# Performance work log

Measured on AMD Instinct MI355X. Metric: run time of the kernel, lower is better.

## Reference

```python
import jax, jax.numpy as jnp
import numpy as np

DN = ('NCHW', 'OIHW', 'NCHW')
LAP = jnp.array([[0., -1., 0.], [-1., 4., -1.], [0., -1., 0.]], dtype=jnp.float32).reshape(1, 1, 3, 3)
CH, NE = 24, 256


def conv(x, w, stride=1, pad=0):
    return jax.lax.conv_general_dilated(x, w, (stride, stride), ((pad, pad), (pad, pad)), dimension_numbers=DN)


def conv_t(x, w):
    # torch ConvTranspose2d(k=4, s=2, p=1); w is torch layout [in, out, 4, 4]
    wt = jnp.flip(w, (2, 3)).transpose(1, 0, 2, 3)
    return jax.lax.conv_general_dilated(x, wt, (1, 1), ((2, 2), (2, 2)), lhs_dilation=(2, 2), dimension_numbers=DN)


def spatial_attn(x, w_sa):
    y = jnp.concatenate([jnp.mean(x, 1, keepdims=True), jnp.max(x, 1, keepdims=True)], 1)
    return x * jax.nn.sigmoid(conv(y, w_sa, pad=3))


def res_branch(x, wr, wp, wsa):
    k = wr.shape[-1]
    h = conv(x, wr, pad=k // 2)
    h = conv(h, wp)
    return jax.nn.relu(spatial_attn(h, wsa))


def enc_block(x, wr, wp, wsa, wout):
    x = x + res_branch(x, wr, wp, wsa)
    return conv(x, wout, stride=2, pad=1)


def dec_block(x, wr, wp, wsa, wout):
    x = conv_t(x, wout)
    return x + res_branch(x, wr, wp, wsa)


def quantize(inp, embed):
    # inp: [B,H,W,D] tokens, embed: [D,N] codebook
    f = inp.reshape(-1, inp.shape[-1])
    dist = (f * f).sum(1, keepdims=True) - 2.0 * (f @ embed) + (embed * embed).sum(0, keepdims=True)
    ind = jnp.argmin(dist, axis=1)
    q = jnp.take(embed.T, ind, axis=0).reshape(inp.shape)
    diff = jnp.mean((jax.lax.stop_gradient(q) - inp) ** 2)
    q = inp + jax.lax.stop_gradient(q - inp)  # straight-through
    return q, diff


def _forward(x, w_img_in, w_img_out,
             w_res_et, w_pw_et, w_sa_et, w_out_et,
             w_res_em, w_pw_em, w_sa_em, w_out_em,
             w_res_ed, w_pw_ed, w_sa_ed, w_out_ed,
             w_res_dt, w_pw_dt, w_sa_dt, w_out_dt,
             w_res_dm, w_pw_dm, w_sa_dm, w_out_dm,
             w_res_dd, w_pw_dd, w_sa_dd, w_out_dd,
             w_squ1, w_squ2, embed2, embed3):
    xl = jax.lax.stop_gradient(conv(jnp.mean(x, 1, keepdims=True), LAP, pad=1))
    h = conv(xl, w_img_in)
    enc1 = enc_block(h, w_res_et, w_pw_et, w_sa_et, w_out_et)      # H/2
    enc2 = enc_block(enc1, w_res_em, w_pw_em, w_sa_em, w_out_em)   # H/4
    enc3 = enc_block(enc2, w_res_ed, w_pw_ed, w_sa_ed, w_out_ed)   # H/8
    qt2, d2 = quantize(enc2.transpose(0, 2, 3, 1), embed2)
    qt2 = qt2.transpose(0, 3, 1, 2)
    qt3, d3 = quantize(enc3.transpose(0, 2, 3, 1), embed3)
    qt3 = qt3.transpose(0, 3, 1, 2)
    dec3 = dec_block(qt3, w_res_dd, w_pw_dd, w_sa_dd, w_out_dd)    # H/4
    dec2 = conv(jnp.concatenate([dec3, qt2], 1), w_squ2)
    dec2 = dec_block(dec2, w_res_dm, w_pw_dm, w_sa_dm, w_out_dm)   # H/2
    dec1 = conv(jnp.concatenate([dec2, enc1], 1), w_squ1)
    dec1 = dec_block(dec1, w_res_dt, w_pw_dt, w_sa_dt, w_out_dt)   # H
    mask_lap = conv(dec1, w_img_out)
    clean_lap = xl - mask_lap
    return mask_lap, clean_lap, (d2 + d3).reshape(1)


def _param_shapes():
    shapes = {'w_img_in': (CH, 1, 1, 1), 'w_img_out': (1, CH, 1, 1),
              'w_squ1': (CH, 2 * CH, 1, 1), 'w_squ2': (CH, 2 * CH, 1, 1),
              'embed2': (CH, NE), 'embed3': (CH, NE)}
    for tag, k in [('et', 7), ('em', 5), ('ed', 3), ('dt', 7), ('dm', 5), ('dd', 3)]:
        shapes['w_res_' + tag] = (CH, CH, k, k)
        shapes['w_pw_' + tag] = (CH, CH, 1, 1)
        shapes['w_sa_' + tag] = (1, 2, 7, 7)
        shapes['w_out_' + tag] = (CH, CH, 4, 4)
    return shapes


def setup_inputs() -> dict:
    key = jax.random.key(0)
    shapes = _param_shapes()
    names = sorted(shapes)
    keys = jax.random.split(key, len(names) + 1)
    inputs = {'x': jax.random.normal(keys[0], (8, 3, 512, 512), dtype=jnp.float32)}
    for k_, name in zip(keys[1:], names):
        w = jax.random.normal(k_, shapes[name], dtype=jnp.float32)
        if not name.startswith('embed'):
            w = w * 0.05  # conv weight init scale
        inputs[name] = w
    return inputs


def reference(x, embed2, embed3, w_img_in, w_img_out,
              w_out_dd, w_out_dm, w_out_dt, w_out_ed, w_out_em, w_out_et,
              w_pw_dd, w_pw_dm, w_pw_dt, w_pw_ed, w_pw_em, w_pw_et,
              w_res_dd, w_res_dm, w_res_dt, w_res_ed, w_res_em, w_res_et,
              w_sa_dd, w_sa_dm, w_sa_dt, w_sa_ed, w_sa_em, w_sa_et,
              w_squ1, w_squ2):
    return _forward(x, w_img_in, w_img_out,
                    w_res_et, w_pw_et, w_sa_et, w_out_et,
                    w_res_em, w_pw_em, w_sa_em, w_out_em,
                    w_res_ed, w_pw_ed, w_sa_ed, w_out_ed,
                    w_res_dt, w_pw_dt, w_sa_dt, w_out_dt,
                    w_res_dm, w_pw_dm, w_sa_dm, w_out_dm,
                    w_res_dd, w_pw_dd, w_sa_dd, w_out_dd,
                    w_squ1, w_squ2, embed2, embed3)
```

## Files before the change

### kernel.cpp

```cpp
#include <hip/hip_runtime.h>
#include <math.h>

#define CH 24

typedef __attribute__((ext_vector_type(8))) short short8v;
typedef __attribute__((ext_vector_type(4))) float f32x4;
typedef unsigned short ushort_t;
typedef unsigned int uint_t;

__device__ inline ushort_t bf16r(float f){
  uint_t u = __float_as_uint(f);
  u += 0x7FFF + ((u>>16)&1);
  return (ushort_t)(u>>16);
}
__device__ inline float bf2f(uint_t u){ return __uint_as_float(u<<16); }

__global__ void k_r_pw(const float* __restrict__ w, float* __restrict__ wT, int CIN){
  int i = blockIdx.x*256 + threadIdx.x;
  if (i >= CIN*24) return;
  int co = i % 24, ci = i/24;
  wT[i] = w[co*CIN+ci];
}
__global__ void k_rmfma(const float* __restrict__ w, ushort_t* __restrict__ wb, int K){
  int i = blockIdx.x*256 + threadIdx.x;
  int n = K*K*1024; if (i >= n) return;
  int j = i & 7, l = (i>>3) & 63, t = (i>>9) & 1, tap = i >> 10;
  int ci = (l>>4)*8 + j, co = t*16 + (l&15);
  int ky = tap / K, kx = tap % K;
  float v = (ci<24 && co<24) ? w[((co*24+ci)*K+ky)*K+kx] : 0.f;
  wb[i] = bf16r(v);
}
__global__ void k_rmfma4(const float* __restrict__ w, ushort_t* __restrict__ wb){
  int i = blockIdx.x*256 + threadIdx.x;
  if (i >= 16384) return;
  int j = i & 7, l = (i>>3) & 63, t = (i>>9) & 1, tap = i >> 10;
  int ci = (l>>4)*8 + j, co = t*16 + (l&15);
  int ky = tap >> 2, kx = tap & 3;
  float v = (ci<24 && co<24) ? w[((ci*24+co)*4+ky)*4+kx] : 0.f;
  wb[i] = bf16r(v);
}


__global__ void k_lap(const float* __restrict__ x, float* __restrict__ xl, int H, int W){
  int idx = blockIdx.x*256 + threadIdx.x;
  int HW = H*W;
  if (idx >= HW) return;
  const float* xb = x + (size_t)blockIdx.z*3*HW;
  float* xo = xl + (size_t)blockIdx.z*HW;
  int px = idx % W, py = idx / W;
#define MEANV(yy,xx) (((yy)>=0&&(yy)<H&&(xx)>=0&&(xx)<W) ? (xb[(yy)*W+(xx)]+xb[HW+(yy)*W+(xx)]+xb[2*HW+(yy)*W+(xx)])*(1.f/3.f) : 0.f)
  float v = 4.f*MEANV(py,px) - MEANV(py-1,px) - MEANV(py+1,px) - MEANV(py,px-1) - MEANV(py,px+1);
#undef MEANV
  xo[idx] = v;
}

template<int K, bool EXPAND, bool INBF, bool OUTBF>
__launch_bounds__(512)
__global__ void k_conv_mfma(const void* in, const ushort_t* __restrict__ wb,
                            const ushort_t* __restrict__ wbpw, const float* __restrict__ wexp,
                            void* out, float* __restrict__ mm,
                            int H, int W, int istrIn, int istrOut, int istrMM){
  constexpr int SW_T = 32 + K - 1;
  constexpr int SH = 16 + K - 1;
  constexpr int NPX = SH*SW_T;
  __shared__ ushort_t lds[NPX*24];
  __shared__ uint_t sc[8][16*20];
  int tid = threadIdx.x;
  const float* inb_f = (const float*)in + (size_t)blockIdx.z*istrIn;
  const ushort_t* inb_b = (const ushort_t*)in + (size_t)blockIdx.z*istrIn;
  int x0g = blockIdx.x*32 - K/2, y0g = blockIdx.y*16 - K/2;
  int HW = H*W;
  for (int i = tid; i < NPX*3; i += 512){
    int q = i / NPX;
    int pp = i - q*NPX;
    int row = pp / SW_T, col = pp - row*SW_T;
    int gy = y0g + row, gx = x0g + col;
    uint4 w4; w4.x=0u; w4.y=0u; w4.z=0u; w4.w=0u;
    if (gy >= 0 && gy < H && gx >= 0 && gx < W){
      size_t base = (size_t)gy*W + gx;
      int c0 = q*8;
      if (EXPAND){
        float val = inb_f[base];
        w4.x = (uint_t)bf16r(val*wexp[c0+0]) | ((uint_t)bf16r(val*wexp[c0+1])<<16);
        w4.y = (uint_t)bf16r(val*wexp[c0+2]) | ((uint_t)bf16r(val*wexp[c0+3])<<16);
        w4.z = (uint_t)bf16r(val*wexp[c0+4]) | ((uint_t)bf16r(val*wexp[c0+5])<<16);
        w4.w = (uint_t)bf16r(val*wexp[c0+6]) | ((uint_t)bf16r(val*wexp[c0+7])<<16);
      } else if (INBF){
        uint_t u0=inb_b[(size_t)(c0+0)*HW+base], u1=inb_b[(size_t)(c0+1)*HW+base];
        uint_t u2=inb_b[(size_t)(c0+2)*HW+base], u3=inb_b[(size_t)(c0+3)*HW+base];
        uint_t u4=inb_b[(size_t)(c0+4)*HW+base], u5=inb_b[(size_t)(c0+5)*HW+base];
        uint_t u6=inb_b[(size_t)(c0+6)*HW+base], u7=inb_b[(size_t)(c0+7)*HW+base];
        w4.x = u0 | (u1<<16); w4.y = u2 | (u3<<16); w4.z = u4 | (u5<<16); w4.w = u6 | (u7<<16);
      } else {
        w4.x = (uint_t)bf16r(inb_f[(size_t)(c0+0)*HW+base]) | ((uint_t)bf16r(inb_f[(size_t)(c0+1)*HW+base])<<16);
        w4.y = (uint_t)bf16r(inb_f[(size_t)(c0+2)*HW+base]) | ((uint_t)bf16r(inb_f[(size_t)(c0+3)*HW+base])<<16);
        w4.z = (uint_t)bf16r(inb_f[(size_t)(c0+4)*HW+base]) | ((uint_t)bf16r(inb_f[(size_t)(c0+5)*HW+base])<<16);
        w4.w = (uint_t)bf16r(inb_f[(size_t)(c0+6)*HW+base]) | ((uint_t)bf16r(inb_f[(size_t)(c0+7)*HW+base])<<16);
      }
    }
    *(uint4*)(lds + (size_t)pp*24 + q*8) = w4;
  }
  __syncthreads();
  int l = tid & 63, wid = tid >> 6;
  int kg = l >> 4, li = l & 15;
  int kgc = (kg < 3) ? kg : 2;
  f32x4 zero = {0.f,0.f,0.f,0.f};
  f32x4 acc[4][2];
  #pragma unroll
  for (int i=0;i<4;i++){ acc[i][0]=zero; acc[i][1]=zero; }

  const ushort_t* aln = lds + li*24 + kgc*8 + (size_t)wid*SW_T*24;

  #pragma unroll
  for (int ky=0; ky<K; ky++){
    #pragma unroll
    for (int kx=0; kx<K; kx++){
      int tap = ky*K + kx;
      const ushort_t* wp = wb + (size_t)tap*1024;
      short8v b0 = *(const short8v*)(wp + l*8);
      short8v b1 = *(const short8v*)(wp + 512 + l*8);
      #pragma unroll
      for (int i=0;i<4;i++){
        const ushort_t* ap = aln + (((i&1)*8 + ky)*SW_T + (i>>1)*16 + kx)*24;
        short8v a = *(const short8v*)ap;
        acc[i][0] = __builtin_amdgcn_mfma_f32_16x16x32_bf16(a, b0, acc[i][0], 0, 0, 0);
        acc[i][1] = __builtin_amdgcn_mfma_f32_16x16x32_bf16(a, b1, acc[i][1], 0, 0, 0);
      }
    }
  }
  short8v bpw0 = *(const short8v*)(wbpw + l*8);
  short8v bpw1 = *(const short8v*)(wbpw + 512 + l*8);
  uint_t* s = sc[wid];
  float* outb_f = (float*)out + (size_t)blockIdx.z*istrOut;
  ushort_t* outb_b = (ushort_t*)out + (size_t)blockIdx.z*istrOut;
  float* mmb = mm + (size_t)blockIdx.z*istrMM;
  #pragma unroll 1
  for (int i=0;i<4;i++){
    __asm__ volatile("s_waitcnt lgkmcnt(0)" ::: "memory");
    __builtin_amdgcn_sched_barrier(0);
    #pragma unroll
    for (int reg=0; reg<4; reg++){
      float v0 = acc[i][0][reg], v1 = acc[i][1][reg];
      float v0n = __shfl_xor(v0, 1, 64);
      float v1n = __shfl_xor(v1, 1, 64);
      int pxr = kg*4 + reg;
      uint_t packed; int uidx;
      if ((li & 1) == 0){
        packed = (uint_t)bf16r(v0) | ((uint_t)bf16r(v0n) << 16);
        uidx = li >> 1;
      } else {
        packed = (uint_t)bf16r(v1n) | ((uint_t)bf16r(v1) << 16);
        uidx = 8 + (li >> 1);
      }
      s[pxr*20 + uidx] = packed;
    }
    __asm__ volatile("s_waitcnt lgkmcnt(0)" ::: "memory");
    __builtin_amdgcn_sched_barrier(0);
    short8v a2 = *(const short8v*)((const ushort_t*)s + li*40 + kg*8);
    f32x4 d0 = __builtin_amdgcn_mfma_f32_16x16x32_bf16(a2, bpw0, zero, 0, 0, 0);
    f32x4 d1 = __builtin_amdgcn_mfma_f32_16x16x32_bf16(a2, bpw1, zero, 0, 0, 0);
    int gy = blockIdx.y*16 + wid + (i&1)*8;
    int gx = blockIdx.x*32 + (i>>1)*16 + kg*4;
    if (OUTBF){
      uint2 p0; p0.x = (uint_t)bf16r(d0[0]) | ((uint_t)bf16r(d0[1])<<16);
      p0.y = (uint_t)bf16r(d0[2]) | ((uint_t)bf16r(d0[3])<<16);
      *(uint2*)(outb_b + (size_t)li*HW + (size_t)gy*W + gx) = p0;
      if (li < 8){
        uint2 p1; p1.x = (uint_t)bf16r(d1[0]) | ((uint_t)bf16r(d1[1])<<16);
        p1.y = (uint_t)bf16r(d1[2]) | ((uint_t)bf16r(d1[3])<<16);
        *(uint2*)(outb_b + (size_t)(16+li)*HW + (size_t)gy*W + gx) = p1;
      }
    } else {
      *(f32x4*)(outb_f + (size_t)li*HW + (size_t)gy*W + gx) = d0;
      if (li < 8)
        *(f32x4*)(outb_f + (size_t)(16+li)*HW + (size_t)gy*W + gx) = d1;
    }
    f32x4 sm, mx;
    #pragma unroll
    for (int reg=0; reg<4; reg++){
      sm[reg] = d0[reg] + d1[reg];
      mx[reg] = fmaxf(d0[reg], (li<8) ? d1[reg] : -3.4e38f);
    }
    #pragma unroll
    for (int m=1; m<16; m<<=1){
      #pragma unroll
      for (int reg=0; reg<4; reg++){
        sm[reg] += __shfl_xor(sm[reg], m, 64);
        mx[reg] = fmaxf(mx[reg], __shfl_xor(mx[reg], m, 64));
      }
    }
    if (li == 0){
      f32x4 me; me[0]=sm[0]*(1.f/24.f); me[1]=sm[1]*(1.f/24.f); me[2]=sm[2]*(1.f/24.f); me[3]=sm[3]*(1.f/24.f);
      *(f32x4*)(mmb + (size_t)gy*W + gx) = me;
      *(f32x4*)(mmb + (size_t)HW + (size_t)gy*W + gx) = mx;
    }
  }
}

template<bool INBF, bool OUTBF>
__launch_bounds__(512)
__global__ void k_convT_mfma(const void* in, const ushort_t* __restrict__ wb,
                             void* out, int Ho, int Wo, int istrIn, int istrOut){
  const int Hi = Ho>>1, Wi = Wo>>1;
  constexpr int SW_T = 18, NPX = 180;
  __shared__ ushort_t lds[NPX*24];
  int tid = threadIdx.x;
  const float* inb_f = (const float*)in + (size_t)blockIdx.z*istrIn;
  const ushort_t* inb_b = (const ushort_t*)in + (size_t)blockIdx.z*istrIn;
  int X0 = blockIdx.x*32, Y0 = blockIdx.y*16;
  int ix0 = (X0>>1) - 1, iy0 = (Y0>>1) - 1;
  int HWi = Hi*Wi;
  for (int i = tid; i < NPX*3; i += 512){
    int q = i / NPX;
    int pp = i - q*NPX;
    int row = pp / SW_T, col = pp - row*SW_T;
    int gy = iy0 + row, gx = ix0 + col;
    uint4 w4; w4.x=0u; w4.y=0u; w4.z=0u; w4.w=0u;
    if (gy>=0 && gy<Hi && gx>=0 && gx<Wi){
      size_t base = (size_t)gy*Wi + gx;
      int c0 = q*8;
      if (INBF){
        uint_t u0=inb_b[(size_t)(c0+0)*HWi+base], u1=inb_b[(size_t)(c0+1)*HWi+base];
        uint_t u2=inb_b[(size_t)(c0+2)*HWi+base], u3=inb_b[(size_t)(c0+3)*HWi+base];
        uint_t u4=inb_b[(size_t)(c0+4)*HWi+base], u5=inb_b[(size_t)(c0+5)*HWi+base];
        uint_t u6=inb_b[(size_t)(c0+6)*HWi+base], u7=inb_b[(size_t)(c0+7)*HWi+base];
        w4.x = u0 | (u1<<16); w4.y = u2 | (u3<<16); w4.z = u4 | (u5<<16); w4.w = u6 | (u7<<16);
      } else {
        w4.x = (uint_t)bf16r(inb_f[(size_t)(c0+0)*HWi+base]) | ((uint_t)bf16r(inb_f[(size_t)(c0+1)*HWi+base])<<16);
        w4.y = (uint_t)bf16r(inb_f[(size_t)(c0+2)*HWi+base]) | ((uint_t)bf16r(inb_f[(size_t)(c0+3)*HWi+base])<<16);
        w4.z = (uint_t)bf16r(inb_f[(size_t)(c0+4)*HWi+base]) | ((uint_t)bf16r(inb_f[(size_t)(c0+5)*HWi+base])<<16);
        w4.w = (uint_t)bf16r(inb_f[(size_t)(c0+6)*HWi+base]) | ((uint_t)bf16r(inb_f[(size_t)(c0+7)*HWi+base])<<16);
      }
    }
    *(uint4*)(lds + (size_t)pp*24 + q*8) = w4;
  }
  __syncthreads();
  int l = tid & 63, wid = tid >> 6;
  int kg = l >> 4, li = l & 15;
  int kgc = (kg < 3) ? kg : 2;
  f32x4 zero = {0.f,0.f,0.f,0.f};
  f32x4 acc[4][2];
  #pragma unroll
  for (int i=0;i<4;i++){ acc[i][0]=zero; acc[i][1]=zero; }

  const ushort_t* aln = lds + li*24 + kgc*8;

  #pragma unroll
  for (int i=0;i<4;i++){
    int g = wid + 8*i;
    int r = g & 15, q = g >> 4;
    int ky0 = (r+1)&1;
    #pragma unroll
    for (int t2=0;t2<2;t2++){
      int ky = ky0 + 2*t2;
      int liy = ((r+1-ky)>>1) + 1;
      #pragma unroll
      for (int u=0;u<2;u++){
        int kx = (q ? 0 : 1) + 2*u;
        int lixb = ((q+1-kx)>>1) + 1;
        int tap = ky*4 + kx;
        const ushort_t* wp = wb + (size_t)tap*1024;
        short8v b0 = *(const short8v*)(wp + l*8);
        short8v b1 = *(const short8v*)(wp + 512 + l*8);
        short8v a = *(const short8v*)(aln + (liy*SW_T + lixb)*24);
        acc[i][0] = __builtin_amdgcn_mfma_f32_16x16x32_bf16(a, b0, acc[i][0], 0, 0, 0);
        acc[i][1] = __builtin_amdgcn_mfma_f32_16x16x32_bf16(a, b1, acc[i][1], 0, 0, 0);
      }
    }
  }
  float* outb_f = (float*)out + (size_t)blockIdx.z*istrOut;
  ushort_t* outb_b = (ushort_t*)out + (size_t)blockIdx.z*istrOut;
  int HWo = Ho*Wo;
  #pragma unroll
  for (int i=0;i<4;i++){
    int g = wid + 8*i;
    int r = g & 15, q = g >> 4;
    int oy = Y0 + r;
    #pragma unroll
    for (int reg=0; reg<4; reg++){
      int ox = X0 + 2*(kg*4 + reg) + q;
      if (OUTBF){
        outb_b[(size_t)li*HWo + (size_t)oy*Wo + ox] = bf16r(acc[i][0][reg]);
        if (li < 8)
          outb_b[(size_t)(16+li)*HWo + (size_t)oy*Wo + ox] = bf16r(acc[i][1][reg]);
      } else {
        outb_f[(size_t)li*HWo + (size_t)oy*Wo + ox] = acc[i][0][reg];
        if (li < 8)
          outb_f[(size_t)(16+li)*HWo + (size_t)oy*Wo + ox] = acc[i][1][reg];
      }
    }
  }
}

template<bool INBF, bool OUTBF>
__launch_bounds__(512)
__global__ void k_down_mfma(const void* in, const ushort_t* __restrict__ wb,
                            void* out, int Ho, int Wo, int istrIn, int istrOut){
  const int Hi = Ho*2, Wi = Wo*2;
  constexpr int NPX = 18*34;
  __shared__ ushort_t lds[NPX*24];
  int tid = threadIdx.x;
  const float* inb_f = (const float*)in + (size_t)blockIdx.z*istrIn;
  const ushort_t* inb_b = (const ushort_t*)in + (size_t)blockIdx.z*istrIn;
  int X0 = blockIdx.x*16, Y0 = blockIdx.y*8;
  int ix0 = 2*X0 - 1, iy0 = 2*Y0 - 1;
  int HWi = Hi*Wi;
  for (int i = tid; i < NPX*3; i += 512){
    int q = i / NPX;
    int pp = i - q*NPX;
    int row = pp / 34;
    int rem = pp - row*34;
    int par = (rem >= 17) ? 1 : 0;
    int sub = rem - par*17;
    int gx = ix0 + 2*sub + par;
    int gy = iy0 + row;
    uint4 w4; w4.x=0u; w4.y=0u; w4.z=0u; w4.w=0u;
    if (gy>=0 && gy<Hi && gx>=0 && gx<Wi){
      size_t base = (size_t)gy*Wi + gx;
      int c0 = q*8;
      if (INBF){
        uint_t u0=inb_b[(size_t)(c0+0)*HWi+base], u1=inb_b[(size_t)(c0+1)*HWi+base];
        uint_t u2=inb_b[(size_t)(c0+2)*HWi+base], u3=inb_b[(size_t)(c0+3)*HWi+base];
        uint_t u4=inb_b[(size_t)(c0+4)*HWi+base], u5=inb_b[(size_t)(c0+5)*HWi+base];
        uint_t u6=inb_b[(size_t)(c0+6)*HWi+base], u7=inb_b[(size_t)(c0+7)*HWi+base];
        w4.x = u0 | (u1<<16); w4.y = u2 | (u3<<16); w4.z = u4 | (u5<<16); w4.w = u6 | (u7<<16);
      } else {
        w4.x = (uint_t)bf16r(inb_f[(size_t)(c0+0)*HWi+base]) | ((uint_t)bf16r(inb_f[(size_t)(c0+1)*HWi+base])<<16);
        w4.y = (uint_t)bf16r(inb_f[(size_t)(c0+2)*HWi+base]) | ((uint_t)bf16r(inb_f[(size_t)(c0+3)*HWi+base])<<16);
        w4.z = (uint_t)bf16r(inb_f[(size_t)(c0+4)*HWi+base]) | ((uint_t)bf16r(inb_f[(size_t)(c0+5)*HWi+base])<<16);
        w4.w = (uint_t)bf16r(inb_f[(size_t)(c0+6)*HWi+base]) | ((uint_t)bf16r(inb_f[(size_t)(c0+7)*HWi+base])<<16);
      }
    }
    *(uint4*)(lds + (size_t)pp*24 + q*8) = w4;
  }
  __syncthreads();
  int l = tid & 63, wid = tid >> 6;
  int kg = l >> 4, li = l & 15;
  int kgc = (kg < 3) ? kg : 2;
  f32x4 zero = {0.f,0.f,0.f,0.f};
  f32x4 acc0 = zero, acc1 = zero;
  const ushort_t* aln = lds + li*24 + kgc*8 + (size_t)(2*wid)*34*24;
  #pragma unroll
  for (int ky=0; ky<4; ky++){
    #pragma unroll
    for (int kx=0; kx<4; kx++){
      int tap = ky*4 + kx;
      const ushort_t* wp = wb + (size_t)tap*1024;
      short8v b0 = *(const short8v*)(wp + l*8);
      short8v b1 = *(const short8v*)(wp + 512 + l*8);
      short8v a = *(const short8v*)(aln + (ky*34 + (kx&1)*17 + (kx>>1))*24);
      acc0 = __builtin_amdgcn_mfma_f32_16x16x32_bf16(a, b0, acc0, 0, 0, 0);
      acc1 = __builtin_amdgcn_mfma_f32_16x16x32_bf16(a, b1, acc1, 0, 0, 0);
    }
  }
  int HWo = Ho*Wo;
  int oy = Y0 + wid, ox = X0 + kg*4;
  if (OUTBF){
    ushort_t* outb = (ushort_t*)out + (size_t)blockIdx.z*istrOut;
    uint2 p0; p0.x = (uint_t)bf16r(acc0[0]) | ((uint_t)bf16r(acc0[1])<<16);
    p0.y = (uint_t)bf16r(acc0[2]) | ((uint_t)bf16r(acc0[3])<<16);
    *(uint2*)(outb + (size_t)li*HWo + (size_t)oy*Wo + ox) = p0;
    if (li < 8){
      uint2 p1; p1.x = (uint_t)bf16r(acc1[0]) | ((uint_t)bf16r(acc1[1])<<16);
      p1.y = (uint_t)bf16r(acc1[2]) | ((uint_t)bf16r(acc1[3])<<16);
      *(uint2*)(outb + (size_t)(16+li)*HWo + (size_t)oy*Wo + ox) = p1;
    }
  } else {
    float* outb = (float*)out + (size_t)blockIdx.z*istrOut;
    *(f32x4*)(outb + (size_t)li*HWo + (size_t)oy*Wo + ox) = acc0;
    if (li < 8)
      *(f32x4*)(outb + (size_t)(16+li)*HWo + (size_t)oy*Wo + ox) = acc1;
  }
}

template<bool BF>
__global__ void k_attn_res(const void* R_, const float* __restrict__ M,
                           const void* X_, const float* __restrict__ wsa,
                           void* out_, int H, int W, int istr, int istrMM){
  int p = (blockIdx.x*256 + threadIdx.x)*4;
  int HW = H*W;
  if (p >= HW) return;
  int py = p / W, px0 = p % W;
  const float* Mb = M + (size_t)blockIdx.z*istrMM;
  float s[4]={0,0,0,0};
  #pragma unroll
  for (int cc=0;cc<2;cc++){
    const float* Mc = Mb + (size_t)cc*HW;
    #pragma unroll 1
    for (int ky=0;ky<7;ky++){
      int gy = py+ky-3;
      if (gy<0||gy>=H) continue;
      const float* mr = Mc + (size_t)gy*W;
      float mv[10];
      #pragma unroll
      for (int j=0;j<10;j++){
        int gx = px0-3+j;
        mv[j] = (gx>=0 && gx<W) ? mr[gx] : 0.f;
      }
      const float* wr = wsa + (cc*7+ky)*7;
      #pragma unroll
      for (int kx=0;kx<7;kx++){
        float wv = wr[kx];
        #pragma unroll
        for (int px=0;px<4;px++) s[px] = fmaf(mv[kx+px], wv, s[px]);
      }
    }
  }
  float g[4];
  #pragma unroll
  for (int px=0;px<4;px++) g[px] = 1.f/(1.f+expf(-s[px]));
  #pragma unroll
  for (int c=0;c<CH;c++){
    float r0,r1,r2,r3, x0v,x1v,x2v,x3v;
    if (BF){
      const ushort_t* Rb = (const ushort_t*)R_ + (size_t)blockIdx.z*istr + (size_t)c*HW + p;
      const ushort_t* Xb = (const ushort_t*)X_ + (size_t)blockIdx.z*istr + (size_t)c*HW + p;
      uint2 rv = *(const uint2*)Rb;
      uint2 xv = *(const uint2*)Xb;
      r0=bf2f(rv.x&0xffffu); r1=bf2f(rv.x>>16); r2=bf2f(rv.y&0xffffu); r3=bf2f(rv.y>>16);
      x0v=bf2f(xv.x&0xffffu); x1v=bf2f(xv.x>>16); x2v=bf2f(xv.y&0xffffu); x3v=bf2f(xv.y>>16);
    } else {
      const float* Rb = (const float*)R_ + (size_t)blockIdx.z*istr + (size_t)c*HW + p;
      const float* Xb = (const float*)X_ + (size_t)blockIdx.z*istr + (size_t)c*HW + p;
      float4 rv = *(const float4*)Rb;
      float4 xv = *(const float4*)Xb;
      r0=rv.x; r1=rv.y; r2=rv.z; r3=rv.w;
      x0v=xv.x; x1v=xv.y; x2v=xv.z; x3v=xv.w;
    }
    float o0 = x0v + fmaxf(r0*g[0], 0.f);
    float o1 = x1v + fmaxf(r1*g[1], 0.f);
    float o2 = x2v + fmaxf(r2*g[2], 0.f);
    float o3 = x3v + fmaxf(r3*g[3], 0.f);
    if (BF){
      ushort_t* Ob = (ushort_t*)out_ + (size_t)blockIdx.z*istr + (size_t)c*HW + p;
      uint2 ov;
      ov.x = (uint_t)bf16r(o0) | ((uint_t)bf16r(o1)<<16);
      ov.y = (uint_t)bf16r(o2) | ((uint_t)bf16r(o3)<<16);
      *(uint2*)Ob = ov;
    } else {
      float* Ob = (float*)out_ + (size_t)blockIdx.z*istr + (size_t)c*HW + p;
      float4 ov; ov.x=o0; ov.y=o1; ov.z=o2; ov.w=o3;
      *(float4*)Ob = ov;
    }
  }
}

template<bool BF>
__global__ void k_attn_res_x(const void* R_, const float* __restrict__ M,
                             const float* __restrict__ XL, const float* __restrict__ wsa,
                             const float* __restrict__ wexp,
                             void* out_, int H, int W, int istr, int istrMM){
  int p = (blockIdx.x*256 + threadIdx.x)*4;
  int HW = H*W;
  if (p >= HW) return;
  int py = p / W, px0 = p % W;
  const float* Mb = M + (size_t)blockIdx.z*istrMM;
  float s[4]={0,0,0,0};
  #pragma unroll
  for (int cc=0;cc<2;cc++){
    const float* Mc = Mb + (size_t)cc*HW;
    #pragma unroll 1
    for (int ky=0;ky<7;ky++){
      int gy = py+ky-3;
      if (gy<0||gy>=H) continue;
      const float* mr = Mc + (size_t)gy*W;
      float mv[10];
      #pragma unroll
      for (int j=0;j<10;j++){
        int gx = px0-3+j;
        mv[j] = (gx>=0 && gx<W) ? mr[gx] : 0.f;
      }
      const float* wr = wsa + (cc*7+ky)*7;
      #pragma unroll
      for (int kx=0;kx<7;kx++){
        float wv = wr[kx];
        #pragma unroll
        for (int px=0;px<4;px++) s[px] = fmaf(mv[kx+px], wv, s[px]);
      }
    }
  }
  float g[4];
  #pragma unroll
  for (int px=0;px<4;px++) g[px] = 1.f/(1.f+expf(-s[px]));
  float4 xl4 = *(const float4*)(XL + (size_t)blockIdx.z*HW + p);
  #pragma unroll
  for (int c=0;c<CH;c++){
    float wc = wexp[c];
    float r0,r1,r2,r3;
    if (BF){
      const ushort_t* Rb = (const ushort_t*)R_ + (size_t)blockIdx.z*istr + (size_t)c*HW + p;
      uint2 rv = *(const uint2*)Rb;
      r0=bf2f(rv.x&0xffffu); r1=bf2f(rv.x>>16); r2=bf2f(rv.y&0xffffu); r3=bf2f(rv.y>>16);
    } else {
      const float* Rb = (const float*)R_ + (size_t)blockIdx.z*istr + (size_t)c*HW + p;
      float4 rv = *(const float4*)Rb;
      r0=rv.x; r1=rv.y; r2=rv.z; r3=rv.w;
    }
    float o0 = xl4.x*wc + fmaxf(r0*g[0], 0.f);
    float o1 = xl4.y*wc + fmaxf(r1*g[1], 0.f);
    float o2 = xl4.z*wc + fmaxf(r2*g[2], 0.f);
    float o3 = xl4.w*wc + fmaxf(r3*g[3], 0.f);
    if (BF){
      ushort_t* Ob = (ushort_t*)out_ + (size_t)blockIdx.z*istr + (size_t)c*HW + p;
      uint2 ov;
      ov.x = (uint_t)bf16r(o0) | ((uint_t)bf16r(o1)<<16);
      ov.y = (uint_t)bf16r(o2) | ((uint_t)bf16r(o3)<<16);
      *(uint2*)Ob = ov;
    } else {
      float* Ob = (float*)out_ + (size_t)blockIdx.z*istr + (size_t)c*HW + p;
      float4 ov; ov.x=o0; ov.y=o1; ov.z=o2; ov.w=o3;
      *(float4*)Ob = ov;
    }
  }
}

__global__ void k_attn_final(const ushort_t* __restrict__ R, const float* __restrict__ M,
                             const ushort_t* __restrict__ X, const float* __restrict__ wsa,
                             const float* __restrict__ wout, const float* __restrict__ xl,
                             float* __restrict__ outMask, float* __restrict__ outClean,
                             int H, int W, int istr, int istrMM){
  int p = (blockIdx.x*256 + threadIdx.x)*4;
  int HW = H*W;
  if (p >= HW) return;
  int py = p / W, px0 = p % W;
  const float* Mb = M + (size_t)blockIdx.z*istrMM;
  float s[4]={0,0,0,0};
  #pragma unroll
  for (int cc=0;cc<2;cc++){
    const float* Mc = Mb + (size_t)cc*HW;
    #pragma unroll 1
    for (int ky=0;ky<7;ky++){
      int gy = py+ky-3;
      if (gy<0||gy>=H) continue;
      const float* mr = Mc + (size_t)gy*W;
      float mv[10];
      #pragma unroll
      for (int j=0;j<10;j++){
        int gx = px0-3+j;
        mv[j] = (gx>=0 && gx<W) ? mr[gx] : 0.f;
      }
      const float* wr = wsa + (cc*7+ky)*7;
      #pragma unroll
      for (int kx=0;kx<7;kx++){
        float wv = wr[kx];
        #pragma unroll
        for (int px=0;px<4;px++) s[px] = fmaf(mv[kx+px], wv, s[px]);
      }
    }
  }
  float g[4];
  #pragma unroll
  for (int px=0;px<4;px++) g[px] = 1.f/(1.f+expf(-s[px]));
  float m0=0.f,m1=0.f,m2=0.f,m3=0.f;
  #pragma unroll
  for (int c=0;c<CH;c++){
    const ushort_t* Rb = R + (size_t)blockIdx.z*istr + (size_t)c*HW + p;
    const ushort_t* Xb = X + (size_t)blockIdx.z*istr + (size_t)c*HW + p;
    uint2 rv = *(const uint2*)Rb;
    uint2 xv = *(const uint2*)Xb;
    float wc = wout[c];
    float o0 = bf2f(xv.x&0xffffu) + fmaxf(bf2f(rv.x&0xffffu)*g[0], 0.f);
    float o1 = bf2f(xv.x>>16)     + fmaxf(bf2f(rv.x>>16)*g[1], 0.f);
    float o2 = bf2f(xv.y&0xffffu) + fmaxf(bf2f(rv.y&0xffffu)*g[2], 0.f);
    float o3 = bf2f(xv.y>>16)     + fmaxf(bf2f(rv.y>>16)*g[3], 0.f);
    m0 = fmaf(o0,wc,m0); m1 = fmaf(o1,wc,m1); m2 = fmaf(o2,wc,m2); m3 = fmaf(o3,wc,m3);
  }
  float4 xlv = *(const float4*)(xl + (size_t)blockIdx.z*HW + p);
  float4 mo; mo.x=m0; mo.y=m1; mo.z=m2; mo.w=m3;
  float4 co; co.x=xlv.x-m0; co.y=xlv.y-m1; co.z=xlv.z-m2; co.w=xlv.w-m3;
  *(float4*)(outMask + (size_t)blockIdx.z*HW + p) = mo;
  *(float4*)(outClean + (size_t)blockIdx.z*HW + p) = co;
}

template<bool BF>
__global__ void k_squeeze(const void* inA_, const void* inB_,
                          const float* __restrict__ wT, void* out_, int HW, int istr){
  int p = (blockIdx.x*256 + threadIdx.x)*4;
  if (p >= HW) return;
  float acc[CH][4];
  #pragma unroll
  for (int co=0;co<CH;co++){ acc[co][0]=0;acc[co][1]=0;acc[co][2]=0;acc[co][3]=0; }
  #pragma unroll 1
  for (int ci=0;ci<48;ci++){
    float v0,v1,v2,v3;
    if (BF){
      const ushort_t* src = (ci<24)
        ? ((const ushort_t*)inA_ + (size_t)blockIdx.z*istr + (size_t)ci*HW + p)
        : ((const ushort_t*)inB_ + (size_t)blockIdx.z*istr + (size_t)(ci-24)*HW + p);
      uint2 rv = *(const uint2*)src;
      v0=bf2f(rv.x&0xffffu); v1=bf2f(rv.x>>16); v2=bf2f(rv.y&0xffffu); v3=bf2f(rv.y>>16);
    } else {
      const float* src = (ci<24)
        ? ((const float*)inA_ + (size_t)blockIdx.z*istr + (size_t)ci*HW + p)
        : ((const float*)inB_ + (size_t)blockIdx.z*istr + (size_t)(ci-24)*HW + p);
      float4 rv = *(const float4*)src;
      v0=rv.x; v1=rv.y; v2=rv.z; v3=rv.w;
    }
    const float* wp = wT + ci*24;
    #pragma unroll
    for (int co=0;co<CH;co++){
      float wv = wp[co];
      acc[co][0] = fmaf(v0, wv, acc[co][0]);
      acc[co][1] = fmaf(v1, wv, acc[co][1]);
      acc[co][2] = fmaf(v2, wv, acc[co][2]);
      acc[co][3] = fmaf(v3, wv, acc[co][3]);
    }
  }
  #pragma unroll
  for (int co=0;co<CH;co++){
    if (BF){
      ushort_t* ob = (ushort_t*)out_ + (size_t)blockIdx.z*istr + (size_t)co*HW + p;
      uint2 ov;
      ov.x = (uint_t)bf16r(acc[co][0]) | ((uint_t)bf16r(acc[co][1])<<16);
      ov.y = (uint_t)bf16r(acc[co][2]) | ((uint_t)bf16r(acc[co][3])<<16);
      *(uint2*)ob = ov;
    } else {
      float* ob = (float*)out_ + (size_t)blockIdx.z*istr + (size_t)co*HW + p;
      float4 o; o.x=acc[co][0]; o.y=acc[co][1]; o.z=acc[co][2]; o.w=acc[co][3];
      *(float4*)ob = o;
    }
  }
}

__global__ void k_quant(const float* __restrict__ enc, const float* __restrict__ embed,
                        float* __restrict__ qt, float* __restrict__ diffAcc, int HW, int istr){
  __shared__ float em[256*28];
  __shared__ float red[4];
  {
    int j = threadIdx.x;
    float s = 0.f;
    #pragma unroll
    for (int c=0;c<CH;c++){
      float e = embed[c*256+j];
      em[j*28+c] = -2.0f*e;
      s = fmaf(e,e,s);
    }
    em[j*28+24] = s; em[j*28+25]=0.f; em[j*28+26]=0.f; em[j*28+27]=0.f;
  }
  __syncthreads();
  int p = blockIdx.x*256 + threadIdx.x;
  const float* eb = enc + (size_t)blockIdx.z*istr;
  float f[CH];
  #pragma unroll
  for (int c=0;c<CH;c++) f[c] = eb[(size_t)c*HW + p];
  float best = 3.4e38f; int bj = 0;
  #pragma unroll 1
  for (int j=0;j<256;j++){
    const float4* row = (const float4*)&em[j*28];
    float s = em[j*28+24];
    #pragma unroll
    for (int q4=0;q4<6;q4++){
      float4 r = row[q4];
      s = fmaf(f[q4*4+0], r.x, s);
      s = fmaf(f[q4*4+1], r.y, s);
      s = fmaf(f[q4*4+2], r.z, s);
      s = fmaf(f[q4*4+3], r.w, s);
    }
    if (s < best){ best = s; bj = j; }
  }
  float* qb = qt + (size_t)blockIdx.z*istr;
  float d = 0.f;
  #pragma unroll
  for (int c=0;c<CH;c++){
    float q = embed[c*256+bj];
    qb[(size_t)c*HW + p] = q;
    float e = q - f[c];
    d = fmaf(e,e,d);
  }
  #pragma unroll
  for (int off=32; off>0; off>>=1) d += __shfl_down(d, off, 64);
  int lane = threadIdx.x & 63, wv = threadIdx.x >> 6;
  if (lane==0) red[wv] = d;
  __syncthreads();
  if (threadIdx.x==0) atomicAdd(diffAcc, red[0]+red[1]+red[2]+red[3]);
}

__global__ void k_diff(const float* __restrict__ acc, float* __restrict__ out){
  out[0] = acc[0]*(1.f/3145728.f) + acc[1]*(1.f/786432.f);
}

extern "C" void kernel_launch(void* const* d_in, const int* in_sizes, int n_in,
                              void* d_out, int out_size, void* d_ws, size_t ws_size,
                              hipStream_t stream) {
  const float* x        = (const float*)d_in[0];
  const float* embed2   = (const float*)d_in[1];
  const float* embed3   = (const float*)d_in[2];
  const float* w_img_in = (const float*)d_in[3];
  const float* w_img_out= (const float*)d_in[4];
  const float* w_out_dd = (const float*)d_in[5];
  const float* w_out_dm = (const float*)d_in[6];
  const float* w_out_dt = (const float*)d_in[7];
  const float* w_out_ed = (const float*)d_in[8];
  const float* w_out_em = (const float*)d_in[9];
  const float* w_out_et = (const float*)d_in[10];
  const float* w_pw_dd  = (const float*)d_in[11];
  const float* w_pw_dm  = (const float*)d_in[12];
  const float* w_pw_dt  = (const float*)d_in[13];
  const float* w_pw_ed  = (const float*)d_in[14];
  const float* w_pw_em  = (const float*)d_in[15];
  const float* w_pw_et  = (const float*)d_in[16];
  const float* w_res_dd = (const float*)d_in[17];
  const float* w_res_dm = (const float*)d_in[18];
  const float* w_res_dt = (const float*)d_in[19];
  const float* w_res_ed = (const float*)d_in[20];
  const float* w_res_em = (const float*)d_in[21];
  const float* w_res_et = (const float*)d_in[22];
  const float* w_sa_dd  = (const float*)d_in[23];
  const float* w_sa_dm  = (const float*)d_in[24];
  const float* w_sa_dt  = (const float*)d_in[25];
  const float* w_sa_ed  = (const float*)d_in[26];
  const float* w_sa_em  = (const float*)d_in[27];
  const float* w_sa_et  = (const float*)d_in[28];
  const float* w_squ1   = (const float*)d_in[29];
  const float* w_squ2   = (const float*)d_in[30];
  (void)in_sizes; (void)n_in; (void)out_size;

  const int HW512 = 512*512, HW256 = 256*256, HW128 = 128*128, HW64 = 64*64;
  const int S512 = 24*HW512, S256 = 24*HW256, S128 = 24*HW128, S64 = 24*HW64;

  float* ws = (float*)d_ws;
  float* OUT = (float*)d_out;
  size_t F = ws_size / sizeof(float);

  float* WT      = ws;
  float* wt_squ1 = WT + 154368;
  float* wt_squ2 = WT + 155520;

  ushort_t* WB = (ushort_t*)(ws + 160000);
  ushort_t* wb_et7   = WB;
  ushort_t* wb_dt7   = WB + 50176;
  ushort_t* wb_em5   = WB + 100352;
  ushort_t* wb_dm5   = WB + 125952;
  ushort_t* wb_pw_et = WB + 151552;
  ushort_t* wb_pw_em = WB + 152576;
  ushort_t* wb_pw_dm = WB + 153600;
  ushort_t* wb_pw_dt = WB + 154624;
  ushort_t* wb4_dd   = WB + 155648;
  ushort_t* wb4_dm   = WB + 172032;
  ushort_t* wb4_dt   = WB + 188416;
  ushort_t* wb4d_et  = WB + 204800;
  ushort_t* wb4d_em  = WB + 221184;
  ushort_t* wb4d_ed  = WB + 237568;
  ushort_t* wb_ed3   = WB + 253952;
  ushort_t* wb_dd3   = WB + 263168;
  ushort_t* wb_pw_ed = WB + 272384;
  ushort_t* wb_pw_dd = WB + 273408;

  const size_t ABASE = 300000;

  auto needBatched = [&](size_t CB)->size_t{
    size_t u_f = (CB*(size_t)S512 + 1)/2;
    if ((size_t)4*S256 > u_f) u_f = (size_t)4*S256;
    if ((size_t)8*S128 > u_f) u_f = (size_t)8*S128;
    return ABASE + 2097152 + (size_t)4*S256 + 3145728 + 786432 + CB*524288 + 2*u_f + 2;
  };
  int CB = 0;
  if (F >= needBatched(8)) CB = 8;
  else if (F >= needBatched(4)) CB = 4;
  else if (F >= needBatched(2)) CB = 2;
  const size_t NEED_B = ABASE + 15925250;
  if (CB == 0 && F < NEED_B) return;

  float *XL, *E2, *Q2, *E3, *Q3, *MM, *DIFF, *U1, *U2;
  ushort_t* E1b;
  if (CB > 0){
    size_t off = ABASE;
    size_t u_f = (CB*(size_t)S512 + 1)/2;
    if ((size_t)4*S256 > u_f) u_f = (size_t)4*S256;
    if ((size_t)8*S128 > u_f) u_f = (size_t)8*S128;
    XL = ws + off; off += 2097152;
    E1b = (ushort_t*)(ws + off); off += (size_t)4*S256;
    Q2 = ws + off; off += 3145728;
    Q3 = ws + off; off += 786432;
    MM = ws + off; off += CB*524288;
    U1 = ws + off; off += u_f;
    U2 = ws + off; off += u_f;
    DIFF = ws + off;
    E2 = OUT;
    E3 = OUT + 3145728;
  } else {
    size_t off = ABASE;
    XL = ws + off; off += 262144;
    U1 = ws + off; off += 6291456;
    U2 = ws + off; off += 6291456;
    E1b = (ushort_t*)(ws + off); off += 1572864;
    E2 = ws + off; off += 393216;
    Q2 = ws + off; off += 393216;
    E3 = ws + off; off += 98304;
    Q3 = ws + off; off += 98304;
    MM = ws + off; off += 524288;
    DIFF = ws + off;
  }
  ushort_t* U1b = (ushort_t*)U1;
  ushort_t* U2b = (ushort_t*)U2;

  k_rmfma<<<dim3(196), 256, 0, stream>>>(w_res_et, wb_et7, 7);
  k_rmfma<<<dim3(196), 256, 0, stream>>>(w_res_dt, wb_dt7, 7);
  k_rmfma<<<dim3(100), 256, 0, stream>>>(w_res_em, wb_em5, 5);
  k_rmfma<<<dim3(100), 256, 0, stream>>>(w_res_dm, wb_dm5, 5);
  k_rmfma<<<dim3(36), 256, 0, stream>>>(w_res_ed, wb_ed3, 3);
  k_rmfma<<<dim3(36), 256, 0, stream>>>(w_res_dd, wb_dd3, 3);
  k_rmfma<<<dim3(4), 256, 0, stream>>>(w_pw_et, wb_pw_et, 1);
  k_rmfma<<<dim3(4), 256, 0, stream>>>(w_pw_em, wb_pw_em, 1);
  k_rmfma<<<dim3(4), 256, 0, stream>>>(w_pw_dm, wb_pw_dm, 1);
  k_rmfma<<<dim3(4), 256, 0, stream>>>(w_pw_dt, wb_pw_dt, 1);
  k_rmfma<<<dim3(4), 256, 0, stream>>>(w_pw_ed, wb_pw_ed, 1);
  k_rmfma<<<dim3(4), 256, 0, stream>>>(w_pw_dd, wb_pw_dd, 1);
  k_rmfma4<<<dim3(64), 256, 0, stream>>>(w_out_dd, wb4_dd);
  k_rmfma4<<<dim3(64), 256, 0, stream>>>(w_out_dm, wb4_dm);
  k_rmfma4<<<dim3(64), 256, 0, stream>>>(w_out_dt, wb4_dt);
  k_rmfma<<<dim3(64), 256, 0, stream>>>(w_out_et, wb4d_et, 4);
  k_rmfma<<<dim3(64), 256, 0, stream>>>(w_out_em, wb4d_em, 4);
  k_rmfma<<<dim3(64), 256, 0, stream>>>(w_out_ed, wb4d_ed, 4);
  k_r_pw<<<dim3(5), 256, 0, stream>>>(w_squ1, wt_squ1, 48);
  k_r_pw<<<dim3(5), 256, 0, stream>>>(w_squ2, wt_squ2, 48);

  hipMemsetAsync(DIFF, 0, 2*sizeof(float), stream);

  auto phase1 = [&](int c0, int nz, float* XLp, ushort_t* E1p){
    k_lap<<<dim3(HW512/256,1,nz), 256, 0, stream>>>(x + (size_t)c0*3*HW512, XLp, 512, 512);
    k_conv_mfma<7,true,false,true><<<dim3(16,32,nz), 512, 0, stream>>>(
        XLp, wb_et7, wb_pw_et, w_img_in, U2b, MM, 512, 512, HW512, S512, 2*HW512);
    k_attn_res_x<true><<<dim3(HW512/1024,1,nz), 256, 0, stream>>>(
        U2b, MM, XLp, w_sa_et, w_img_in, U1b, 512, 512, S512, 2*HW512);
    k_down_mfma<true,true><<<dim3(16,32,nz), 512, 0, stream>>>(U1b, wb4d_et, E1p, 256, 256, S512, S256);
  };

  auto deep = [&](int nb, ushort_t* E1p, float* SAp, float* SBp, float* E2p, float* Q2p,
                  float* E3p, float* Q3p, float* MMp, ushort_t* D1p){
    ushort_t* SAb = (ushort_t*)SAp;
    ushort_t* SBb = (ushort_t*)SBp;
    int mm256 = 2*HW256, mm128 = 2*HW128;
    k_conv_mfma<5,false,true,true><<<dim3(8,16,nb), 512, 0, stream>>>(
        E1p, wb_em5, wb_pw_em, nullptr, SAb, MMp, 256, 256, S256, S256, mm256);
    k_attn_res<true><<<dim3(HW256/1024,1,nb), 256, 0, stream>>>(SAb, MMp, E1p, w_sa_em, SBb, 256, 256, S256, mm256);
    k_down_mfma<true,false><<<dim3(8,16,nb), 512, 0, stream>>>(SBb, wb4d_em, E2p, 128, 128, S256, S128);
    k_conv_mfma<3,false,false,false><<<dim3(4,8,nb), 512, 0, stream>>>(
        E2p, wb_ed3, wb_pw_ed, nullptr, SAp, MMp, 128, 128, S128, S128, mm128);
    k_attn_res<false><<<dim3(HW128/1024,1,nb), 256, 0, stream>>>(SAp, MMp, E2p, w_sa_ed, SBp, 128, 128, S128, mm128);
    k_down_mfma<false,false><<<dim3(4,8,nb), 512, 0, stream>>>(SBp, wb4d_ed, E3p, 64, 64, S128, S64);
    k_quant<<<dim3(HW128/256,1,nb), 256, 0, stream>>>(E2p, embed2, Q2p, DIFF+0, HW128, S128);
    k_quant<<<dim3(HW64/256,1,nb), 256, 0, stream>>>(E3p, embed3, Q3p, DIFF+1, HW64, S64);
    k_convT_mfma<false,false><<<dim3(4,8,nb), 512, 0, stream>>>(Q3p, wb4_dd, SAp, 128, 128, S64, S128);
    k_conv_mfma<3,false,false,false><<<dim3(4,8,nb), 512, 0, stream>>>(
        SAp, wb_dd3, wb_pw_dd, nullptr, SBp, MMp, 128, 128, S128, S128, mm128);
    k_attn_res<false><<<dim3(HW128/1024,1,nb), 256, 0, stream>>>(SBp, MMp, SAp, w_sa_dd, SAp, 128, 128, S128, mm128);
    k_squeeze<false><<<dim3(HW128/1024,1,nb), 256, 0, stream>>>(SAp, Q2p, wt_squ2, SBp, HW128, S128);
    k_convT_mfma<false,true><<<dim3(8,16,nb), 512, 0, stream>>>(SBp, wb4_dm, SAb, 256, 256, S128, S256);
    k_conv_mfma<5,false,true,true><<<dim3(8,16,nb), 512, 0, stream>>>(
        SAb, wb_dm5, wb_pw_dm, nullptr, SBb, MMp, 256, 256, S256, S256, mm256);
    k_attn_res<true><<<dim3(HW256/1024,1,nb), 256, 0, stream>>>(SBb, MMp, SAb, w_sa_dm, SAb, 256, 256, S256, mm256);
    k_squeeze<true><<<dim3(HW256/1024,1,nb), 256, 0, stream>>>(SAb, E1p, wt_squ1, D1p, HW256, S256);
  };

  auto phase3 = [&](int c0, int nz, const ushort_t* D1p, const float* XLp){
    k_convT_mfma<true,true><<<dim3(16,32,nz), 512, 0, stream>>>(D1p, wb4_dt, U1b, 512, 512, S256, S512);
    k_conv_mfma<7,false,true,true><<<dim3(16,32,nz), 512, 0, stream>>>(
        U1b, wb_dt7, wb_pw_dt, nullptr, U2b, MM, 512, 512, S512, S512, 2*HW512);
    k_attn_final<<<dim3(HW512/1024,1,nz), 256, 0, stream>>>(
        U2b, MM, U1b, w_sa_dt, w_img_out, XLp,
        OUT + (size_t)c0*HW512, OUT + 2097152 + (size_t)c0*HW512,
        512, 512, S512, 2*HW512);
  };

  if (CB > 0){
    for (int c0=0;c0<8;c0+=CB)
      phase1(c0, CB, XL + (size_t)c0*HW512, E1b + (size_t)c0*S256);
    deep(8, E1b, U1, U2, E2, Q2, E3, Q3, MM, E1b);
    for (int c0=0;c0<8;c0+=CB)
      phase3(c0, CB, E1b + (size_t)c0*S256, XL + (size_t)c0*HW512);
  } else {
    for (int b=0;b<8;b++){
      phase1(b, 1, XL, E1b);
      deep(1, E1b, U1, U2, E2, Q2, E3, Q3, MM, (ushort_t*)U2);
      phase3(b, 1, (ushort_t*)U2, XL);
    }
  }

  k_diff<<<1, 1, 0, stream>>>(DIFF, OUT + 4194304);
}
```

Baseline: 1.311 ms.

## Merge weight reorder launches, fold channel mean into pointwise MFMA, alias LDS scratch

Replaces twenty small weight-reordering kernel launches with a single k_reorder kernel that dispatches on block index. The pointwise weights get an extra output column holding the mean over output channels, so the channel mean comes straight out of the MFMA (lane 8 of d1). This drops the shuffle-based sum reduction. The separate shared scratch array is removed and the input tile LDS is reused after a barrier, lowering LDS use per block and possibly raising occupancy. The trade-off is the extra __syncthreads and a bf16-rounded mean weight, which differs slightly from the fp32 sum.

```diff
diff --git a/kernel.cpp b/kernel.cpp
--- a/kernel.cpp
+++ b/kernel.cpp
@@ -15,14 +15,15 @@
 }
 __device__ inline float bf2f(uint_t u){ return __uint_as_float(u<<16); }
 
-__global__ void k_r_pw(const float* __restrict__ w, float* __restrict__ wT, int CIN){
-  int i = blockIdx.x*256 + threadIdx.x;
-  if (i >= CIN*24) return;
-  int co = i % 24, ci = i/24;
-  wT[i] = w[co*CIN+ci];
-}
-__global__ void k_rmfma(const float* __restrict__ w, ushort_t* __restrict__ wb, int K){
-  int i = blockIdx.x*256 + threadIdx.x;
+struct WPtrs {
+  const float *res_et, *res_dt, *res_em, *res_dm, *res_ed, *res_dd;
+  const float *pw_et, *pw_em, *pw_dm, *pw_dt, *pw_ed, *pw_dd;
+  const float *out_dd, *out_dm, *out_dt;
+  const float *out_et, *out_em, *out_ed;
+  const float *squ1, *squ2;
+};
+
+__device__ inline void do_rmfma(const float* w, ushort_t* wb, int K, int i){
   int n = K*K*1024; if (i >= n) return;
   int j = i & 7, l = (i>>3) & 63, t = (i>>9) & 1, tap = i >> 10;
   int ci = (l>>4)*8 + j, co = t*16 + (l&15);
@@ -30,14 +31,58 @@
   float v = (ci<24 && co<24) ? w[((co*24+ci)*K+ky)*K+kx] : 0.f;
   wb[i] = bf16r(v);
 }
-__global__ void k_rmfma4(const float* __restrict__ w, ushort_t* __restrict__ wb){
-  int i = blockIdx.x*256 + threadIdx.x;
+__device__ inline void do_rmfma_pw(const float* w, ushort_t* wb, int i){
+  if (i >= 1024) return;
+  int j = i & 7, l = (i>>3) & 63, t = (i>>9) & 1;
+  int ci = (l>>4)*8 + j, co = t*16 + (l&15);
+  float v = 0.f;
+  if (ci < 24){
+    if (co < 24) v = w[co*24+ci];
+    else if (co == 24){
+      float s = 0.f;
+      for (int c2=0;c2<24;c2++) s += w[c2*24+ci];
+      v = s*(1.f/24.f);
+    }
+  }
+  wb[i] = bf16r(v);
+}
+__device__ inline void do_rmfma4(const float* w, ushort_t* wb, int i){
   if (i >= 16384) return;
   int j = i & 7, l = (i>>3) & 63, t = (i>>9) & 1, tap = i >> 10;
   int ci = (l>>4)*8 + j, co = t*16 + (l&15);
   int ky = tap >> 2, kx = tap & 3;
   float v = (ci<24 && co<24) ? w[((ci*24+co)*4+ky)*4+kx] : 0.f;
   wb[i] = bf16r(v);
+}
+__device__ inline void do_rpw48(const float* w, float* wT, int i){
+  if (i >= 1152) return;
+  int co = i % 24, ci = i/24;
+  wT[i] = w[co*48+ci];
+}
+
+__global__ void k_reorder(WPtrs P, ushort_t* __restrict__ WB,
+                          float* __restrict__ wt_squ1, float* __restrict__ wt_squ2){
+  int b = blockIdx.x, t = threadIdx.x;
+  if      (b < 196)  do_rmfma(P.res_et, WB+0,      7, b*256+t);
+  else if (b < 392)  do_rmfma(P.res_dt, WB+50176,  7, (b-196)*256+t);
+  else if (b < 492)  do_rmfma(P.res_em, WB+100352, 5, (b-392)*256+t);
+  else if (b < 592)  do_rmfma(P.res_dm, WB+125952, 5, (b-492)*256+t);
+  else if (b < 628)  do_rmfma(P.res_ed, WB+253952, 3, (b-592)*256+t);
+  else if (b < 664)  do_rmfma(P.res_dd, WB+263168, 3, (b-628)*256+t);
+  else if (b < 668)  do_rmfma_pw(P.pw_et, WB+151552, (b-664)*256+t);
+  else if (b < 672)  do_rmfma_pw(P.pw_em, WB+152576, (b-668)*256+t);
+  else if (b < 676)  do_rmfma_pw(P.pw_dm, WB+153600, (b-672)*256+t);
+  else if (b < 680)  do_rmfma_pw(P.pw_dt, WB+154624, (b-676)*256+t);
+  else if (b < 684)  do_rmfma_pw(P.pw_ed, WB+272384, (b-680)*256+t);
+  else if (b < 688)  do_rmfma_pw(P.pw_dd, WB+273408, (b-684)*256+t);
+  else if (b < 752)  do_rmfma4(P.out_dd, WB+155648, (b-688)*256+t);
+  else if (b < 816)  do_rmfma4(P.out_dm, WB+172032, (b-752)*256+t);
+  else if (b < 880)  do_rmfma4(P.out_dt, WB+188416, (b-816)*256+t);
+  else if (b < 944)  do_rmfma(P.out_et, WB+204800, 4, (b-880)*256+t);
+  else if (b < 1008) do_rmfma(P.out_em, WB+221184, 4, (b-944)*256+t);
+  else if (b < 1072) do_rmfma(P.out_ed, WB+237568, 4, (b-1008)*256+t);
+  else if (b < 1077) do_rpw48(P.squ1, wt_squ1, (b-1072)*256+t);
+  else if (b < 1082) do_rpw48(P.squ2, wt_squ2, (b-1077)*256+t);
 }
 
 
@@ -63,8 +108,7 @@
   constexpr int SW_T = 32 + K - 1;
   constexpr int SH = 16 + K - 1;
   constexpr int NPX = SH*SW_T;
-  __shared__ ushort_t lds[NPX*24];
-  __shared__ uint_t sc[8][16*20];
+  __shared__ __align__(16) ushort_t lds[NPX*24];
   int tid = threadIdx.x;
   const float* inb_f = (const float*)in + (size_t)blockIdx.z*istrIn;
   const ushort_t* inb_b = (const ushort_t*)in + (size_t)blockIdx.z*istrIn;
@@ -128,9 +172,10 @@
       }
     }
   }
+  __syncthreads();
   short8v bpw0 = *(const short8v*)(wbpw + l*8);
   short8v bpw1 = *(const short8v*)(wbpw + 512 + l*8);
-  uint_t* s = sc[wid];
+  uint_t* s = (uint_t*)lds + wid*320;
   float* outb_f = (float*)out + (size_t)blockIdx.z*istrOut;
   ushort_t* outb_b = (ushort_t*)out + (size_t)blockIdx.z*istrOut;
   float* mmb = mm + (size_t)blockIdx.z*istrMM;
@@ -175,25 +220,20 @@
       if (li < 8)
         *(f32x4*)(outb_f + (size_t)(16+li)*HW + (size_t)gy*W + gx) = d1;
     }
-    f32x4 sm, mx;
+    f32x4 mx;
     #pragma unroll
-    for (int reg=0; reg<4; reg++){
-      sm[reg] = d0[reg] + d1[reg];
+    for (int reg=0; reg<4; reg++)
       mx[reg] = fmaxf(d0[reg], (li<8) ? d1[reg] : -3.4e38f);
-    }
     #pragma unroll
     for (int m=1; m<16; m<<=1){
       #pragma unroll
-      for (int reg=0; reg<4; reg++){
-        sm[reg] += __shfl_xor(sm[reg], m, 64);
+      for (int reg=0; reg<4; reg++)
         mx[reg] = fmaxf(mx[reg], __shfl_xor(mx[reg], m, 64));
-      }
-    }
-    if (li == 0){
-      f32x4 me; me[0]=sm[0]*(1.f/24.f); me[1]=sm[1]*(1.f/24.f); me[2]=sm[2]*(1.f/24.f); me[3]=sm[3]*(1.f/24.f);
-      *(f32x4*)(mmb + (size_t)gy*W + gx) = me;
+    }
+    if (li == 8)
+      *(f32x4*)(mmb + (size_t)gy*W + gx) = d1;
+    if (li == 0)
       *(f32x4*)(mmb + (size_t)HW + (size_t)gy*W + gx) = mx;
-    }
   }
 }
 
@@ -203,7 +243,7 @@
                              void* out, int Ho, int Wo, int istrIn, int istrOut){
   const int Hi = Ho>>1, Wi = Wo>>1;
   constexpr int SW_T = 18, NPX = 180;
-  __shared__ ushort_t lds[NPX*24];
+  __shared__ __align__(16) ushort_t lds[NPX*24];
   int tid = threadIdx.x;
   const float* inb_f = (const float*)in + (size_t)blockIdx.z*istrIn;
   const ushort_t* inb_b = (const ushort_t*)in + (size_t)blockIdx.z*istrIn;
@@ -298,7 +338,7 @@
                             void* out, int Ho, int Wo, int istrIn, int istrOut){
   const int Hi = Ho*2, Wi = Wo*2;
   constexpr int NPX = 18*34;
-  __shared__ ushort_t lds[NPX*24];
+  __shared__ __align__(16) ushort_t lds[NPX*24];
   int tid = threadIdx.x;
   const float* inb_f = (const float*)in + (size_t)blockIdx.z*istrIn;
   const ushort_t* inb_b = (const ushort_t*)in + (size_t)blockIdx.z*istrIn;
@@ -794,26 +834,15 @@
   ushort_t* U1b = (ushort_t*)U1;
   ushort_t* U2b = (ushort_t*)U2;
 
-  k_rmfma<<<dim3(196), 256, 0, stream>>>(w_res_et, wb_et7, 7);
-  k_rmfma<<<dim3(196), 256, 0, stream>>>(w_res_dt, wb_dt7, 7);
-  k_rmfma<<<dim3(100), 256, 0, stream>>>(w_res_em, wb_em5, 5);
-  k_rmfma<<<dim3(100), 256, 0, stream>>>(w_res_dm, wb_dm5, 5);
-  k_rmfma<<<dim3(36), 256, 0, stream>>>(w_res_ed, wb_ed3, 3);
-  k_rmfma<<<dim3(36), 256, 0, stream>>>(w_res_dd, wb_dd3, 3);
-  k_rmfma<<<dim3(4), 256, 0, stream>>>(w_pw_et, wb_pw_et, 1);
-  k_rmfma<<<dim3(4), 256, 0, stream>>>(w_pw_em, wb_pw_em, 1);
-  k_rmfma<<<dim3(4), 256, 0, stream>>>(w_pw_dm, wb_pw_dm, 1);
-  k_rmfma<<<dim3(4), 256, 0, stream>>>(w_pw_dt, wb_pw_dt, 1);
-  k_rmfma<<<dim3(4), 256, 0, stream>>>(w_pw_ed, wb_pw_ed, 1);
-  k_rmfma<<<dim3(4), 256, 0, stream>>>(w_pw_dd, wb_pw_dd, 1);
-  k_rmfma4<<<dim3(64), 256, 0, stream>>>(w_out_dd, wb4_dd);
-  k_rmfma4<<<dim3(64), 256, 0, stream>>>(w_out_dm, wb4_dm);
-  k_rmfma4<<<dim3(64), 256, 0, stream>>>(w_out_dt, wb4_dt);
-  k_rmfma<<<dim3(64), 256, 0, stream>>>(w_out_et, wb4d_et, 4);
-  k_rmfma<<<dim3(64), 256, 0, stream>>>(w_out_em, wb4d_em, 4);
-  k_rmfma<<<dim3(64), 256, 0, stream>>>(w_out_ed, wb4d_ed, 4);
-  k_r_pw<<<dim3(5), 256, 0, stream>>>(w_squ1, wt_squ1, 48);
-  k_r_pw<<<dim3(5), 256, 0, stream>>>(w_squ2, wt_squ2, 48);
+  WPtrs P;
+  P.res_et=w_res_et; P.res_dt=w_res_dt; P.res_em=w_res_em; P.res_dm=w_res_dm;
+  P.res_ed=w_res_ed; P.res_dd=w_res_dd;
+  P.pw_et=w_pw_et; P.pw_em=w_pw_em; P.pw_dm=w_pw_dm; P.pw_dt=w_pw_dt;
+  P.pw_ed=w_pw_ed; P.pw_dd=w_pw_dd;
+  P.out_dd=w_out_dd; P.out_dm=w_out_dm; P.out_dt=w_out_dt;
+  P.out_et=w_out_et; P.out_em=w_out_em; P.out_ed=w_out_ed;
+  P.squ1=w_squ1; P.squ2=w_squ2;
+  k_reorder<<<dim3(1082), 256, 0, stream>>>(P, WB, wt_squ1, wt_squ2);
 
   hipMemsetAsync(DIFF, 0, 2*sizeof(float), stream);
 
```

Result: faster. 1.269 ms (-3.2%).
